# Performance work log

Hardware: AMD Instinct MI355X
Metric: run time of the kernel (lower is better)

Reference implementation:

```python
import jax, jax.numpy as jnp
import numpy as np

N_NODES = 100_000
N_EDGES = 1_250_000
IN_CH = 64
HID = 64
OUT_CH = 10
K = 5
NUM_GRAPHS = 64


def setup_inputs() -> dict:
    key = jax.random.key(0)
    ks = jax.random.split(key, 8)
    x = jax.random.normal(ks[0], (N_NODES, IN_CH), dtype=jnp.float32)
    edge_index = jax.random.randint(ks[1], (2, N_EDGES), 0, N_NODES)
    batch = jnp.sort(jax.random.randint(ks[2], (N_NODES,), 0, NUM_GRAPHS))
    s_in = float(1.0 / np.sqrt(IN_CH))
    s_h = float(1.0 / np.sqrt(HID))
    W1 = jax.random.uniform(ks[3], (K, IN_CH, HID), minval=-s_in, maxval=s_in, dtype=jnp.float32)
    b1 = jnp.zeros((HID,), jnp.float32)
    W2 = jax.random.uniform(ks[4], (K, HID, HID), minval=-s_h, maxval=s_h, dtype=jnp.float32)
    b2 = jnp.zeros((HID,), jnp.float32)
    Wfc = jax.random.uniform(ks[5], (HID, OUT_CH), minval=-s_h, maxval=s_h, dtype=jnp.float32)
    bfc = jnp.zeros((OUT_CH,), jnp.float32)
    return dict(x=x, edge_index=edge_index, batch=batch,
                W1=W1, b1=b1, W2=W2, b2=b2, Wfc=Wfc, bfc=bfc)


def _cheb_conv(x, src, dst, W, b):
    """PyG ChebConv with normalization='rw', lambda_max=2.
    L_rw = I - D^{-1} A ; scaled L_hat = 2*L/lambda_max - I = -D^{-1}A
    (self-loop weights cancel to 0), so each hop is a weighted scatter-add."""
    n = x.shape[0]
    deg = jax.ops.segment_sum(jnp.ones((src.shape[0],), x.dtype), src, num_segments=n)
    inv_deg = jnp.where(deg > 0, 1.0 / deg, 0.0)
    ew = -inv_deg[src]  # per-edge weight of L_hat

    def prop(t):  # (L_hat t)[i] = sum_{j->i} ew * t[j]
        return jax.ops.segment_sum(ew[:, None] * t[src], dst, num_segments=n)

    Tx0 = x
    out = Tx0 @ W[0]
    Tx1 = prop(Tx0)
    out = out + Tx1 @ W[1]
    for k in range(2, W.shape[0]):
        Tx2 = 2.0 * prop(Tx1) - Tx0
        out = out + Tx2 @ W[k]
        Tx0, Tx1 = Tx1, Tx2
    return out + b


def reference(x, edge_index, batch, W1, b1, W2, b2, Wfc, bfc):
    src, dst = edge_index[0], edge_index[1]
    h = jax.nn.selu(_cheb_conv(x, src, dst, W1, b1))
    # AlphaDropout is identity at inference
    h = jax.nn.selu(_cheb_conv(h, src, dst, W2, b2))
    g = jax.ops.segment_sum(h, batch, num_segments=NUM_GRAPHS)  # global_add_pool
    return g @ Wfc + bfc
```

## Files before the change

kernel.cpp:

```cpp
#include <hip/hip_runtime.h>
#include <cstdint>

#define CH 64
#define NBLK 256
#define NBMAX 1024
#define SRCMASK 0x1FFFFu

typedef __attribute__((ext_vector_type(8))) short bf16x8;
typedef __attribute__((ext_vector_type(8))) unsigned short u16x8;
typedef __attribute__((ext_vector_type(4))) float f32x4;
typedef unsigned int uint32;
typedef unsigned char uchar;

__device__ __forceinline__ unsigned short f2bf(float x) {
  unsigned u = __float_as_uint(x);
  u += 0x7FFF + ((u >> 16) & 1);
  return (unsigned short)(u >> 16);
}
__device__ __forceinline__ float bflo(uint32 u) { return __uint_as_float(u << 16); }
__device__ __forceinline__ float bfhi(uint32 u) { return __uint_as_float(u & 0xFFFF0000u); }
__device__ __forceinline__ uint32 bfpack(float lo, float hi) {
  return ((uint32)f2bf(hi) << 16) | (uint32)f2bf(lo);
}

__global__ __launch_bounds__(256) void k_b1(const int* __restrict__ src, const int* __restrict__ dst,
                                            int* __restrict__ cntD, int* __restrict__ cntS, int E, int NB) {
  __shared__ int hD[NBMAX], hS[NBMAX];
  int t = threadIdx.x, b = blockIdx.x;
  for (int i = t; i < NBMAX; i += 256) { hD[i] = 0; hS[i] = 0; }
  __syncthreads();
  int chunk = (E + NBLK - 1) / NBLK;
  int e0 = b * chunk, e1 = min(E, e0 + chunk);
  for (int e = e0 + t; e < e1; e += 256) {
    atomicAdd(&hD[dst[e] >> 7], 1);
    atomicAdd(&hS[src[e] >> 7], 1);
  }
  __syncthreads();
  for (int i = t; i < NB; i += 256) {
    cntD[i * NBLK + b] = hD[i];
    cntS[i * NBLK + b] = hS[i];
  }
}

__global__ __launch_bounds__(256) void k_scan_local(const int* __restrict__ in, int* __restrict__ out,
                                                    int* __restrict__ bsum, int total) {
  __shared__ int s[256];
  int t = threadIdx.x;
  int base = blockIdx.x * 1024 + t * 4;
  int v0 = (base + 0 < total) ? in[base + 0] : 0;
  int v1 = (base + 1 < total) ? in[base + 1] : 0;
  int v2 = (base + 2 < total) ? in[base + 2] : 0;
  int v3 = (base + 3 < total) ? in[base + 3] : 0;
  int sum = v0 + v1 + v2 + v3;
  s[t] = sum;
  __syncthreads();
  for (int off = 1; off < 256; off <<= 1) {
    int x = (t >= off) ? s[t - off] : 0;
    __syncthreads();
    s[t] += x;
    __syncthreads();
  }
  int excl = s[t] - sum;
  if (base + 0 < total) out[base + 0] = excl;  excl += v0;
  if (base + 1 < total) out[base + 1] = excl;  excl += v1;
  if (base + 2 < total) out[base + 2] = excl;  excl += v2;
  if (base + 3 < total) out[base + 3] = excl;
  if (t == 255) bsum[blockIdx.x] = s[255];
}

__global__ __launch_bounds__(256) void k_scan_bsums(int* bsum, int nb) {
  __shared__ int s[256];
  int t = threadIdx.x;
  int v = (t < nb) ? bsum[t] : 0;
  s[t] = v;
  __syncthreads();
  for (int off = 1; off < 256; off <<= 1) {
    int x = (t >= off) ? s[t - off] : 0;
    __syncthreads();
    s[t] += x;
    __syncthreads();
  }
  if (t < nb) bsum[t] = s[t] - v;
}

__global__ __launch_bounds__(256) void k_scan_add(int* __restrict__ arr, const int* __restrict__ bsum, int total) {
  int i = blockIdx.x * 256 + threadIdx.x;
  if (i < total) arr[i] += bsum[i >> 10];
}

__global__ __launch_bounds__(256) void k_b2(const int* __restrict__ src, const int* __restrict__ dst,
                                            const int* __restrict__ cbaseD, const int* __restrict__ cbaseS,
                                            uint32* __restrict__ etmp, uchar* __restrict__ svals, int E, int NB) {
  __shared__ int curD[NBMAX], curS[NBMAX];
  int t = threadIdx.x, b = blockIdx.x;
  for (int i = t; i < NB; i += 256) {
    curD[i] = cbaseD[i * NBLK + b];
    curS[i] = cbaseS[i * NBLK + b];
  }
  __syncthreads();
  int chunk = (E + NBLK - 1) / NBLK;
  int e0 = b * chunk, e1 = min(E, e0 + chunk);
  for (int e = e0 + t; e < e1; e += 256) {
    int s = src[e], d = dst[e];
    int pd = atomicAdd(&curD[d >> 7], 1);
    etmp[pd] = ((uint32)(d & 127) << 17) | (uint32)s;
    int ps = atomicAdd(&curS[s >> 7], 1);
    svals[ps] = (uchar)(s & 127);
  }
}

__global__ __launch_bounds__(256) void k_b3_deg(const uchar* __restrict__ svals, const int* __restrict__ cbaseS,
                                                float* __restrict__ neg_inv, int n, int E, int NB) {
  __shared__ int h[128];
  int t = threadIdx.x, k = blockIdx.x;
  if (t < 128) h[t] = 0;
  __syncthreads();
  int lo = cbaseS[k * NBLK];
  int hi = (k + 1 < NB) ? cbaseS[(k + 1) * NBLK] : E;
  for (int e = lo + t; e < hi; e += 256) atomicAdd(&h[svals[e]], 1);
  __syncthreads();
  if (t < 128) {
    int node = k * 128 + t;
    if (node < n) {
      int c = h[t];
      neg_inv[node] = c > 0 ? (-1.0f / (float)c) : 0.0f;
    }
  }
}

__global__ __launch_bounds__(256) void k_b3_dst(const uint32* __restrict__ etmp, const int* __restrict__ cbaseD,
                                                const float* __restrict__ neg_inv, int2* __restrict__ erec,
                                                int* __restrict__ row_ptr, int n, int E, int NB) {
  __shared__ int h[128], sc[128], cur[128];
  int t = threadIdx.x, k = blockIdx.x;
  if (t < 128) h[t] = 0;
  __syncthreads();
  int lo = cbaseD[k * NBLK];
  int hi = (k + 1 < NB) ? cbaseD[(k + 1) * NBLK] : E;
  for (int e = lo + t; e < hi; e += 256) atomicAdd(&h[(etmp[e] >> 17) & 127], 1);
  __syncthreads();
  if (t < 128) sc[t] = h[t];
  __syncthreads();
  for (int off = 1; off < 128; off <<= 1) {
    int x = (t < 128 && t >= off) ? sc[t - off] : 0;
    __syncthreads();
    if (t < 128) sc[t] += x;
    __syncthreads();
  }
  if (t < 128) {
    int excl = sc[t] - h[t];
    cur[t] = excl;
    int node = k * 128 + t;
    if (node < n) row_ptr[node] = lo + excl;
  }
  if (k == NB - 1 && t == 0) row_ptr[n] = E;
  __syncthreads();
  for (int e = lo + t; e < hi; e += 256) {
    uint32 r = etmp[e];
    int s = (int)(r & SRCMASK);
    int pos = atomicAdd(&cur[(r >> 17) & 127], 1);
    erec[lo + pos] = make_int2(s, __float_as_int(neg_inv[s]));
  }
}

__global__ __launch_bounds__(256) void k_cast(const float* __restrict__ x, unsigned short* __restrict__ xb,
                                              int total8) {
  int i = blockIdx.x * 256 + threadIdx.x;
  if (i < total8) {
    const float4* p = (const float4*)(x + (size_t)i * 8);
    float4 v0 = p[0], v1 = p[1];
    u16x8 w;
    w[0] = f2bf(v0.x); w[1] = f2bf(v0.y); w[2] = f2bf(v0.z); w[3] = f2bf(v0.w);
    w[4] = f2bf(v1.x); w[5] = f2bf(v1.y); w[6] = f2bf(v1.z); w[7] = f2bf(v1.w);
    *(u16x8*)(xb + (size_t)i * 8) = w;
  }
}

__global__ __launch_bounds__(256) void k_prop(const int* __restrict__ row_ptr, const int2* __restrict__ erec,
                                              const uint32* __restrict__ t_in,
                                              const uint32* __restrict__ t_sub,
                                              uint32* __restrict__ t_out, int n, int mode) {
  int tid = threadIdx.x;
  int lane = tid & 63;
  int cp = lane & 31;
  int h = lane >> 5;
  int node = blockIdx.x * 8 + ((tid >> 6) << 1) + h;
  bool active = node < n;
  int beg = active ? row_ptr[node] : 0;
  int end = active ? row_ptr[node + 1] : 0;
  float a0 = 0.f, a1 = 0.f, b0 = 0.f, b1 = 0.f, c0 = 0.f, c1 = 0.f, d0 = 0.f, d1 = 0.f;
  float e0a = 0.f, e1a = 0.f, f0 = 0.f, f1 = 0.f, g0 = 0.f, g1 = 0.f, h0 = 0.f, h1 = 0.f;
  int e = beg;
  for (; e + 8 <= end; e += 8) {
    int2 q0 = erec[e + 0]; int2 q1 = erec[e + 1]; int2 q2 = erec[e + 2]; int2 q3 = erec[e + 3];
    int2 q4 = erec[e + 4]; int2 q5 = erec[e + 5]; int2 q6 = erec[e + 6]; int2 q7 = erec[e + 7];
    uint32 u0 = t_in[q0.x * 32 + cp];
    uint32 u1 = t_in[q1.x * 32 + cp];
    uint32 u2 = t_in[q2.x * 32 + cp];
    uint32 u3 = t_in[q3.x * 32 + cp];
    uint32 u4 = t_in[q4.x * 32 + cp];
    uint32 u5 = t_in[q5.x * 32 + cp];
    uint32 u6 = t_in[q6.x * 32 + cp];
    uint32 u7 = t_in[q7.x * 32 + cp];
    float w0 = __int_as_float(q0.y), w1 = __int_as_float(q1.y);
    float w2 = __int_as_float(q2.y), w3 = __int_as_float(q3.y);
    float w4 = __int_as_float(q4.y), w5 = __int_as_float(q5.y);
    float w6 = __int_as_float(q6.y), w7 = __int_as_float(q7.y);
    a0 = fmaf(w0, bflo(u0), a0);   a1 = fmaf(w0, bfhi(u0), a1);
    b0 = fmaf(w1, bflo(u1), b0);   b1 = fmaf(w1, bfhi(u1), b1);
    c0 = fmaf(w2, bflo(u2), c0);   c1 = fmaf(w2, bfhi(u2), c1);
    d0 = fmaf(w3, bflo(u3), d0);   d1 = fmaf(w3, bfhi(u3), d1);
    e0a = fmaf(w4, bflo(u4), e0a); e1a = fmaf(w4, bfhi(u4), e1a);
    f0 = fmaf(w5, bflo(u5), f0);   f1 = fmaf(w5, bfhi(u5), f1);
    g0 = fmaf(w6, bflo(u6), g0);   g1 = fmaf(w6, bfhi(u6), g1);
    h0 = fmaf(w7, bflo(u7), h0);   h1 = fmaf(w7, bfhi(u7), h1);
  }
  if (e + 4 <= end) {
    int2 q0 = erec[e + 0]; int2 q1 = erec[e + 1]; int2 q2 = erec[e + 2]; int2 q3 = erec[e + 3];
    uint32 u0 = t_in[q0.x * 32 + cp];
    uint32 u1 = t_in[q1.x * 32 + cp];
    uint32 u2 = t_in[q2.x * 32 + cp];
    uint32 u3 = t_in[q3.x * 32 + cp];
    float w0 = __int_as_float(q0.y), w1 = __int_as_float(q1.y);
    float w2 = __int_as_float(q2.y), w3 = __int_as_float(q3.y);
    a0 = fmaf(w0, bflo(u0), a0);   a1 = fmaf(w0, bfhi(u0), a1);
    b0 = fmaf(w1, bflo(u1), b0);   b1 = fmaf(w1, bfhi(u1), b1);
    c0 = fmaf(w2, bflo(u2), c0);   c1 = fmaf(w2, bfhi(u2), c1);
    d0 = fmaf(w3, bflo(u3), d0);   d1 = fmaf(w3, bfhi(u3), d1);
    e += 4;
  }
  if (e + 2 <= end) {
    int2 q0 = erec[e + 0]; int2 q1 = erec[e + 1];
    uint32 u0 = t_in[q0.x * 32 + cp];
    uint32 u1 = t_in[q1.x * 32 + cp];
    float w0 = __int_as_float(q0.y), w1 = __int_as_float(q1.y);
    a0 = fmaf(w0, bflo(u0), a0);   a1 = fmaf(w0, bfhi(u0), a1);
    b0 = fmaf(w1, bflo(u1), b0);   b1 = fmaf(w1, bfhi(u1), b1);
    e += 2;
  }
  if (e < end) {
    int2 q = erec[e];
    uint32 u = t_in[q.x * 32 + cp];
    float w = __int_as_float(q.y);
    a0 = fmaf(w, bflo(u), a0);
    a1 = fmaf(w, bfhi(u), a1);
  }
  float s0 = ((a0 + b0) + (c0 + d0)) + ((e0a + f0) + (g0 + h0));
  float s1 = ((a1 + b1) + (c1 + d1)) + ((e1a + f1) + (g1 + h1));
  if (active) {
    if (mode == 2) {
      uint32 u = t_sub[(size_t)node * 32 + cp];
      s0 = 2.0f * s0 - bflo(u);
      s1 = 2.0f * s1 - bfhi(u);
    }
    t_out[(size_t)node * 32 + cp] = bfpack(s0, s1);
  }
}

__global__ __launch_bounds__(256) void k_prepW(const float* __restrict__ W, unsigned short* __restrict__ Wt) {
  int o = blockIdx.x * 256 + threadIdx.x;
  if (o < 64 * 320) {
    int j = o / 320, k = o - j * 320;
    Wt[o] = f2bf(W[k * 64 + j]);
  }
}

__device__ __forceinline__ float selu(float v) {
  const float sc = 1.0507009873554805f, al = 1.6732632423543773f;
  return (v > 0.f) ? (sc * v) : (sc * al * (expf(v) - 1.f));
}

__global__ __launch_bounds__(256) void k_gemm5(
    const unsigned short* __restrict__ M0, const unsigned short* __restrict__ M1,
    const unsigned short* __restrict__ M2, const unsigned short* __restrict__ M3,
    const unsigned short* __restrict__ M4,
    const unsigned short* __restrict__ Wt, const float* __restrict__ bias,
    unsigned short* __restrict__ outp, int n) {
  __shared__ unsigned short lds[32 * 320];
  const int t = threadIdx.x;
  const int lane = t & 63, wave = t >> 6;
  const int node0 = blockIdx.x * 32;
  const unsigned short* mats[5] = {M0, M1, M2, M3, M4};
#pragma unroll
  for (int m = 0; m < 5; ++m) {
    int row = t >> 3;
    int cc = t & 7;
    int ca = m * 8 + cc;
    u16x8 w = {};
    if (node0 + row < n)
      w = *(const u16x8*)(mats[m] + (size_t)(node0 + row) * CH + cc * 8);
    *(u16x8*)(&lds[row * 320 + ((ca ^ (row & 7)) << 3)]) = w;
  }
  __syncthreads();
  const int g = lane >> 4, r16 = lane & 15;
  const int rowA0 = r16, rowA1 = r16 + 16;
  const int colB = wave * 16 + r16;
  f32x4 acc0 = {}, acc1 = {};
#pragma unroll 2
  for (int kk = 0; kk < 10; ++kk) {
    int ca = kk * 4 + g;
    bf16x8 a0 = *(const bf16x8*)(&lds[rowA0 * 320 + ((ca ^ (rowA0 & 7)) << 3)]);
    bf16x8 a1 = *(const bf16x8*)(&lds[rowA1 * 320 + ((ca ^ (rowA1 & 7)) << 3)]);
    bf16x8 b = *(const bf16x8*)(Wt + colB * 320 + kk * 32 + g * 8);
    acc0 = __builtin_amdgcn_mfma_f32_16x16x32_bf16(a0, b, acc0, 0, 0, 0);
    acc1 = __builtin_amdgcn_mfma_f32_16x16x32_bf16(a1, b, acc1, 0, 0, 0);
  }
  const f32x4 accs[2] = {acc0, acc1};
  int col = wave * 16 + r16;
  float bv = bias[col];
#pragma unroll
  for (int i = 0; i < 2; ++i) {
#pragma unroll
    for (int rr = 0; rr < 4; ++rr) {
      int row = node0 + i * 16 + g * 4 + rr;
      if (row < n)
        outp[(size_t)row * CH + col] = f2bf(selu(accs[i][rr] + bv));
    }
  }
}

__global__ __launch_bounds__(256) void k_gemm5_pool(
    const unsigned short* __restrict__ M0, const unsigned short* __restrict__ M1,
    const unsigned short* __restrict__ M2, const unsigned short* __restrict__ M3,
    const unsigned short* __restrict__ M4,
    const unsigned short* __restrict__ Wt, const float* __restrict__ bias,
    const int* __restrict__ batch, float* __restrict__ gout, int n) {
  __shared__ unsigned short lds[32 * 320];
  const int t = threadIdx.x;
  const int lane = t & 63, wave = t >> 6;
  const int node0 = blockIdx.x * 32;
  const unsigned short* mats[5] = {M0, M1, M2, M3, M4};
#pragma unroll
  for (int m = 0; m < 5; ++m) {
    int row = t >> 3;
    int cc = t & 7;
    int ca = m * 8 + cc;
    u16x8 w = {};
    if (node0 + row < n)
      w = *(const u16x8*)(mats[m] + (size_t)(node0 + row) * CH + cc * 8);
    *(u16x8*)(&lds[row * 320 + ((ca ^ (row & 7)) << 3)]) = w;
  }
  __syncthreads();
  const int g = lane >> 4, r16 = lane & 15;
  const int rowA0 = r16, rowA1 = r16 + 16;
  const int colB = wave * 16 + r16;
  f32x4 acc0 = {}, acc1 = {};
#pragma unroll 2
  for (int kk = 0; kk < 10; ++kk) {
    int ca = kk * 4 + g;
    bf16x8 a0 = *(const bf16x8*)(&lds[rowA0 * 320 + ((ca ^ (rowA0 & 7)) << 3)]);
    bf16x8 a1 = *(const bf16x8*)(&lds[rowA1 * 320 + ((ca ^ (rowA1 & 7)) << 3)]);
    bf16x8 b = *(const bf16x8*)(Wt + colB * 320 + kk * 32 + g * 8);
    acc0 = __builtin_amdgcn_mfma_f32_16x16x32_bf16(a0, b, acc0, 0, 0, 0);
    acc1 = __builtin_amdgcn_mfma_f32_16x16x32_bf16(a1, b, acc1, 0, 0, 0);
  }
  __syncthreads();
  float* S = (float*)lds;
  const f32x4 accs[2] = {acc0, acc1};
  {
    int col = wave * 16 + r16;
    float bv = bias[col];
#pragma unroll
    for (int i = 0; i < 2; ++i)
#pragma unroll
      for (int rr = 0; rr < 4; ++rr) {
        int row = i * 16 + g * 4 + rr;
        S[row * 65 + col] = selu(accs[i][rr] + bv);
      }
  }
  __syncthreads();
  int c = t & 63, w = t >> 6;
  float cur = 0.f;
  int curg = -1;
  for (int r = 0; r < 8; ++r) {
    int row = w * 8 + r;
    int gn = node0 + row;
    if (gn >= n) break;
    int b = batch[gn];
    if (b != curg) {
      if (curg >= 0) atomicAdd(&gout[curg * CH + c], cur);
      curg = b;
      cur = 0.f;
    }
    cur += S[row * 65 + c];
  }
  if (curg >= 0) atomicAdd(&gout[curg * CH + c], cur);
}

__global__ __launch_bounds__(256) void k_fc(const float* __restrict__ g, const float* __restrict__ Wfc,
                                            const float* __restrict__ bfc, float* __restrict__ outp,
                                            int ng, int oc) {
  int i = blockIdx.x * 256 + threadIdx.x;
  if (i < ng * oc) {
    int gi = i / oc, o = i - gi * oc;
    float s = bfc[o];
    for (int ci = 0; ci < CH; ++ci) s += g[gi * CH + ci] * Wfc[ci * oc + o];
    outp[i] = s;
  }
}

extern "C" void kernel_launch(void* const* d_in, const int* in_sizes, int n_in,
                              void* d_out, int out_size, void* d_ws, size_t ws_size,
                              hipStream_t stream) {
  const float* x   = (const float*)d_in[0];
  const int* eidx  = (const int*)d_in[1];
  const int* batch = (const int*)d_in[2];
  const float* W1  = (const float*)d_in[3];
  const float* b1  = (const float*)d_in[4];
  const float* W2  = (const float*)d_in[5];
  const float* b2  = (const float*)d_in[6];
  const float* Wfc = (const float*)d_in[7];
  const float* bfc = (const float*)d_in[8];
  float* out = (float*)d_out;

  const int n  = in_sizes[0] / CH;
  const int E  = in_sizes[1] / 2;
  const int OC = in_sizes[8];
  const int NG = out_size / OC;
  const int NB = (n + 127) >> 7;

  const int* src = eidx;
  const int* dst = eidx + E;

  size_t off = 0;
  char* base = (char*)d_ws;
  auto alloc = [&](size_t bytes) -> void* {
    size_t cur = (off + 255) & ~(size_t)255;
    off = cur + bytes;
    return (void*)(base + cur);
  };
  const int scan_total = NB * NBLK;
  const int scan_nb    = (scan_total + 1023) / 1024;
  int*   cntD   = (int*)alloc((size_t)scan_total * 4);
  int*   cntS   = (int*)alloc((size_t)scan_total * 4);
  int*   bsumD  = (int*)alloc((size_t)scan_nb * 4);
  int*   bsumS  = (int*)alloc((size_t)scan_nb * 4);
  float* neg_inv = (float*)alloc((size_t)n * 4);
  int*   row_ptr = (int*)alloc((size_t)(n + 1) * 4);
  int2*  erec    = (int2*)alloc((size_t)E * 8);
  const size_t tb16 = (size_t)n * CH * 2;
  unsigned short* Xb = (unsigned short*)alloc(tb16);
  unsigned short* T1 = (unsigned short*)alloc(tb16);
  unsigned short* T2 = (unsigned short*)alloc(tb16);
  unsigned short* T3 = (unsigned short*)alloc(tb16);
  unsigned short* T4 = (unsigned short*)alloc(tb16);
  unsigned short* H  = (unsigned short*)alloc(tb16);
  uint32* etmp  = (uint32*)alloc((size_t)E * 4);
  uchar*  svals = (uchar*)alloc((size_t)E);
  float* g  = (float*)alloc((size_t)NG * CH * 4);
  unsigned short* Wt1 = (unsigned short*)alloc(64 * 320 * 2);
  unsigned short* Wt2 = (unsigned short*)alloc(64 * 320 * 2);
  if (off > ws_size) return;

  hipMemsetAsync(g, 0, (size_t)NG * CH * 4, stream);

  k_b1<<<NBLK, 256, 0, stream>>>(src, dst, cntD, cntS, E, NB);
  k_scan_local<<<scan_nb, 256, 0, stream>>>(cntD, cntD, bsumD, scan_total);
  k_scan_bsums<<<1, 256, 0, stream>>>(bsumD, scan_nb);
  k_scan_add<<<(scan_total + 255) / 256, 256, 0, stream>>>(cntD, bsumD, scan_total);
  k_scan_local<<<scan_nb, 256, 0, stream>>>(cntS, cntS, bsumS, scan_total);
  k_scan_bsums<<<1, 256, 0, stream>>>(bsumS, scan_nb);
  k_scan_add<<<(scan_total + 255) / 256, 256, 0, stream>>>(cntS, bsumS, scan_total);
  k_b2<<<NBLK, 256, 0, stream>>>(src, dst, cntD, cntS, etmp, svals, E, NB);
  k_b3_deg<<<NB, 256, 0, stream>>>(svals, cntS, neg_inv, n, E, NB);
  k_b3_dst<<<NB, 256, 0, stream>>>(etmp, cntD, neg_inv, erec, row_ptr, n, E, NB);

  k_prepW<<<80, 256, 0, stream>>>(W1, Wt1);
  k_prepW<<<80, 256, 0, stream>>>(W2, Wt2);
  k_cast<<<(n * CH / 8 + 255) / 256, 256, 0, stream>>>(x, Xb, n * CH / 8);

  const int pb = (n + 7) / 8;
  const int gb = (n + 31) / 32;
  k_prop<<<pb, 256, 0, stream>>>(row_ptr, erec, (const uint32*)Xb, nullptr, (uint32*)T1, n, 1);
  k_prop<<<pb, 256, 0, stream>>>(row_ptr, erec, (const uint32*)T1, (const uint32*)Xb, (uint32*)T2, n, 2);
  k_prop<<<pb, 256, 0, stream>>>(row_ptr, erec, (const uint32*)T2, (const uint32*)T1, (uint32*)T3, n, 2);
  k_prop<<<pb, 256, 0, stream>>>(row_ptr, erec, (const uint32*)T3, (const uint32*)T2, (uint32*)T4, n, 2);
  k_gemm5<<<gb, 256, 0, stream>>>(Xb, T1, T2, T3, T4, Wt1, b1, H, n);
  k_prop<<<pb, 256, 0, stream>>>(row_ptr, erec, (const uint32*)H,  nullptr, (uint32*)T1, n, 1);
  k_prop<<<pb, 256, 0, stream>>>(row_ptr, erec, (const uint32*)T1, (const uint32*)H,  (uint32*)T2, n, 2);
  k_prop<<<pb, 256, 0, stream>>>(row_ptr, erec, (const uint32*)T2, (const uint32*)T1, (uint32*)T3, n, 2);
  k_prop<<<pb, 256, 0, stream>>>(row_ptr, erec, (const uint32*)T3, (const uint32*)T2, (uint32*)T4, n, 2);
  k_gemm5_pool<<<gb, 256, 0, stream>>>(H, T1, T2, T3, T4, Wt2, b2, batch, g, n);
  k_fc<<<(NG * OC + 255) / 256, 256, 0, stream>>>(g, Wfc, bfc, out, NG, OC);
}
```

Measured before the change: 417.9 us.

## Process propagation nodes in degree-sorted order for wavefront load balance

Adds a counting sort of nodes by in-degree (histogram, scan, scatter) and has the propagation kernel look up its node through this permutation, so the two nodes sharing a wavefront and the nodes sharing a block have similar edge counts. The aim is to cut divergence and tail imbalance in the eight propagation passes. The cost is three extra small kernels plus a memset, an indirection load per node, and loss of locality in the output writes and row_ptr reads. Within a degree bucket, the atomic scatter leaves node order nondeterministic.

```diff
diff --git a/kernel.cpp b/kernel.cpp
--- a/kernel.cpp
+++ b/kernel.cpp
@@ -163,6 +163,43 @@
   }
 }
 
+__global__ __launch_bounds__(256) void k_deg_hist(const int* __restrict__ row_ptr, int* __restrict__ hist, int n) {
+  __shared__ int h[256];
+  int t = threadIdx.x;
+  h[t] = 0;
+  __syncthreads();
+  for (int i = blockIdx.x * 256 + t; i < n; i += gridDim.x * 256) {
+    int d = min(row_ptr[i + 1] - row_ptr[i], 255);
+    atomicAdd(&h[255 - d], 1);
+  }
+  __syncthreads();
+  if (h[t]) atomicAdd(&hist[t], h[t]);
+}
+
+__global__ __launch_bounds__(256) void k_deg_scan(int* hist) {
+  __shared__ int s[256];
+  int t = threadIdx.x;
+  int v = hist[t];
+  s[t] = v;
+  __syncthreads();
+  for (int off = 1; off < 256; off <<= 1) {
+    int x = (t >= off) ? s[t - off] : 0;
+    __syncthreads();
+    s[t] += x;
+    __syncthreads();
+  }
+  hist[t] = s[t] - v;
+}
+
+__global__ __launch_bounds__(256) void k_deg_scatter(const int* __restrict__ row_ptr, int* __restrict__ hist,
+                                                     int* __restrict__ perm, int n) {
+  for (int i = blockIdx.x * 256 + threadIdx.x; i < n; i += gridDim.x * 256) {
+    int d = min(row_ptr[i + 1] - row_ptr[i], 255);
+    int pos = atomicAdd(&hist[255 - d], 1);
+    perm[pos] = i;
+  }
+}
+
 __global__ __launch_bounds__(256) void k_cast(const float* __restrict__ x, unsigned short* __restrict__ xb,
                                               int total8) {
   int i = blockIdx.x * 256 + threadIdx.x;
@@ -177,6 +214,7 @@
 }
 
 __global__ __launch_bounds__(256) void k_prop(const int* __restrict__ row_ptr, const int2* __restrict__ erec,
+                                              const int* __restrict__ perm,
                                               const uint32* __restrict__ t_in,
                                               const uint32* __restrict__ t_sub,
                                               uint32* __restrict__ t_out, int n, int mode) {
@@ -184,8 +222,9 @@
   int lane = tid & 63;
   int cp = lane & 31;
   int h = lane >> 5;
-  int node = blockIdx.x * 8 + ((tid >> 6) << 1) + h;
-  bool active = node < n;
+  int slot = blockIdx.x * 8 + ((tid >> 6) << 1) + h;
+  bool active = slot < n;
+  int node = active ? perm[slot] : 0;
   int beg = active ? row_ptr[node] : 0;
   int end = active ? row_ptr[node + 1] : 0;
   float a0 = 0.f, a1 = 0.f, b0 = 0.f, b1 = 0.f, c0 = 0.f, c1 = 0.f, d0 = 0.f, d1 = 0.f;
@@ -438,6 +477,8 @@
   float* neg_inv = (float*)alloc((size_t)n * 4);
   int*   row_ptr = (int*)alloc((size_t)(n + 1) * 4);
   int2*  erec    = (int2*)alloc((size_t)E * 8);
+  int*   perm    = (int*)alloc((size_t)n * 4);
+  int*   dhist   = (int*)alloc(256 * 4);
   const size_t tb16 = (size_t)n * CH * 2;
   unsigned short* Xb = (unsigned short*)alloc(tb16);
   unsigned short* T1 = (unsigned short*)alloc(tb16);
@@ -453,6 +494,7 @@
   if (off > ws_size) return;
 
   hipMemsetAsync(g, 0, (size_t)NG * CH * 4, stream);
+  hipMemsetAsync(dhist, 0, 256 * 4, stream);
 
   k_b1<<<NBLK, 256, 0, stream>>>(src, dst, cntD, cntS, E, NB);
   k_scan_local<<<scan_nb, 256, 0, stream>>>(cntD, cntD, bsumD, scan_total);
@@ -464,6 +506,9 @@
   k_b2<<<NBLK, 256, 0, stream>>>(src, dst, cntD, cntS, etmp, svals, E, NB);
   k_b3_deg<<<NB, 256, 0, stream>>>(svals, cntS, neg_inv, n, E, NB);
   k_b3_dst<<<NB, 256, 0, stream>>>(etmp, cntD, neg_inv, erec, row_ptr, n, E, NB);
+  k_deg_hist<<<256, 256, 0, stream>>>(row_ptr, dhist, n);
+  k_deg_scan<<<1, 256, 0, stream>>>(dhist);
+  k_deg_scatter<<<256, 256, 0, stream>>>(row_ptr, dhist, perm, n);
 
   k_prepW<<<80, 256, 0, stream>>>(W1, Wt1);
   k_prepW<<<80, 256, 0, stream>>>(W2, Wt2);
@@ -471,15 +516,15 @@
 
   const int pb = (n + 7) / 8;
   const int gb = (n + 31) / 32;
-  k_prop<<<pb, 256, 0, stream>>>(row_ptr, erec, (const uint32*)Xb, nullptr, (uint32*)T1, n, 1);
-  k_prop<<<pb, 256, 0, stream>>>(row_ptr, erec, (const uint32*)T1, (const uint32*)Xb, (uint32*)T2, n, 2);
-  k_prop<<<pb, 256, 0, stream>>>(row_ptr, erec, (const uint32*)T2, (const uint32*)T1, (uint32*)T3, n, 2);
-  k_prop<<<pb, 256, 0, stream>>>(row_ptr, erec, (const uint32*)T3, (const uint32*)T2, (uint32*)T4, n, 2);
+  k_prop<<<pb, 256, 0, stream>>>(row_ptr, erec, perm, (const uint32*)Xb, nullptr, (uint32*)T1, n, 1);
+  k_prop<<<pb, 256, 0, stream>>>(row_ptr, erec, perm, (const uint32*)T1, (const uint32*)Xb, (uint32*)T2, n, 2);
+  k_prop<<<pb, 256, 0, stream>>>(row_ptr, erec, perm, (const uint32*)T2, (const uint32*)T1, (uint32*)T3, n, 2);
+  k_prop<<<pb, 256, 0, stream>>>(row_ptr, erec, perm, (const uint32*)T3, (const uint32*)T2, (uint32*)T4, n, 2);
   k_gemm5<<<gb, 256, 0, stream>>>(Xb, T1, T2, T3, T4, Wt1, b1, H, n);
-  k_prop<<<pb, 256, 0, stream>>>(row_ptr, erec, (const uint32*)H,  nullptr, (uint32*)T1, n, 1);
-  k_prop<<<pb, 256, 0, stream>>>(row_ptr, erec, (const uint32*)T1, (const uint32*)H,  (uint32*)T2, n, 2);
-  k_prop<<<pb, 256, 0, stream>>>(row_ptr, erec, (const uint32*)T2, (const uint32*)T1, (uint32*)T3, n, 2);
-  k_prop<<<pb, 256, 0, stream>>>(row_ptr, erec, (const uint32*)T3, (const uint32*)T2, (uint32*)T4, n, 2);
+  k_prop<<<pb, 256, 0, stream>>>(row_ptr, erec, perm, (const uint32*)H,  nullptr, (uint32*)T1, n, 1);
+  k_prop<<<pb, 256, 0, stream>>>(row_ptr, erec, perm, (const uint32*)T1, (const uint32*)H,  (uint32*)T2, n, 2);
+  k_prop<<<pb, 256, 0, stream>>>(row_ptr, erec, perm, (const uint32*)T2, (const uint32*)T1, (uint32*)T3, n, 2);
+  k_prop<<<pb, 256, 0, stream>>>(row_ptr, erec, perm, (const uint32*)T3, (const uint32*)T2, (uint32*)T4, n, 2);
   k_gemm5_pool<<<gb, 256, 0, stream>>>(H, T1, T2, T3, T4, Wt2, b2, batch, g, n);
   k_fc<<<(NG * OC + 255) / 256, 256, 0, stream>>>(g, Wfc, bfc, out, NG, OC);
 }
```

Measured after the change: 725.0 us. 1.73x slower.

## Make GEMM kernels persistent with double-buffered LDS and register-resident weights

Applied to the files above, without the earlier changes.

Both Chebyshev GEMM kernels become persistent grid-stride loops over 32-node strips, with at most 1024 blocks. Each wave loads its weight fragments into registers once, and the next strip's five input matrices are loaded into a second LDS buffer while the current strip's MFMAs run. This aims to cut per-block setup cost, avoid re-reading weights every strip, and overlap global loads with compute. In exchange it uses more registers and twice the LDS, which can lower occupancy, and the GEMMs are a small share of total time next to the eight propagation passes.

```diff
diff --git a/kernel.cpp b/kernel.cpp
--- a/kernel.cpp
+++ b/kernel.cpp
@@ -275,47 +275,72 @@
     const unsigned short* __restrict__ M2, const unsigned short* __restrict__ M3,
     const unsigned short* __restrict__ M4,
     const unsigned short* __restrict__ Wt, const float* __restrict__ bias,
-    unsigned short* __restrict__ outp, int n) {
-  __shared__ unsigned short lds[32 * 320];
+    unsigned short* __restrict__ outp, int n, int nstrips) {
+  __shared__ unsigned short lds[2][32 * 320];
   const int t = threadIdx.x;
   const int lane = t & 63, wave = t >> 6;
-  const int node0 = blockIdx.x * 32;
+  const int g = lane >> 4, r16 = lane & 15;
   const unsigned short* mats[5] = {M0, M1, M2, M3, M4};
-#pragma unroll
-  for (int m = 0; m < 5; ++m) {
-    int row = t >> 3;
-    int cc = t & 7;
-    int ca = m * 8 + cc;
-    u16x8 w = {};
-    if (node0 + row < n)
-      w = *(const u16x8*)(mats[m] + (size_t)(node0 + row) * CH + cc * 8);
-    *(u16x8*)(&lds[row * 320 + ((ca ^ (row & 7)) << 3)]) = w;
-  }
-  __syncthreads();
-  const int g = lane >> 4, r16 = lane & 15;
-  const int rowA0 = r16, rowA1 = r16 + 16;
   const int colB = wave * 16 + r16;
-  f32x4 acc0 = {}, acc1 = {};
-#pragma unroll 2
-  for (int kk = 0; kk < 10; ++kk) {
-    int ca = kk * 4 + g;
-    bf16x8 a0 = *(const bf16x8*)(&lds[rowA0 * 320 + ((ca ^ (rowA0 & 7)) << 3)]);
-    bf16x8 a1 = *(const bf16x8*)(&lds[rowA1 * 320 + ((ca ^ (rowA1 & 7)) << 3)]);
-    bf16x8 b = *(const bf16x8*)(Wt + colB * 320 + kk * 32 + g * 8);
-    acc0 = __builtin_amdgcn_mfma_f32_16x16x32_bf16(a0, b, acc0, 0, 0, 0);
-    acc1 = __builtin_amdgcn_mfma_f32_16x16x32_bf16(a1, b, acc1, 0, 0, 0);
-  }
-  const f32x4 accs[2] = {acc0, acc1};
-  int col = wave * 16 + r16;
-  float bv = bias[col];
-#pragma unroll
-  for (int i = 0; i < 2; ++i) {
-#pragma unroll
-    for (int rr = 0; rr < 4; ++rr) {
-      int row = node0 + i * 16 + g * 4 + rr;
-      if (row < n)
-        outp[(size_t)row * CH + col] = f2bf(selu(accs[i][rr] + bv));
-    }
+  bf16x8 Bf[10];
+#pragma unroll
+  for (int kk = 0; kk < 10; ++kk)
+    Bf[kk] = *(const bf16x8*)(Wt + colB * 320 + kk * 32 + g * 8);
+  const float bv = bias[colB];
+  const int srow = t >> 3, scc = t & 7;
+
+  int strip = blockIdx.x;
+  if (strip >= nstrips) return;
+  int cur = 0;
+  {
+    int node0 = strip * 32;
+#pragma unroll
+    for (int m = 0; m < 5; ++m) {
+      int ca = m * 8 + scc;
+      u16x8 w = {};
+      if (node0 + srow < n)
+        w = *(const u16x8*)(mats[m] + (size_t)(node0 + srow) * CH + scc * 8);
+      *(u16x8*)(&lds[0][srow * 320 + ((ca ^ (srow & 7)) << 3)]) = w;
+    }
+  }
+  __syncthreads();
+  for (; strip < nstrips; strip += gridDim.x) {
+    int nxt = strip + gridDim.x;
+    if (nxt < nstrips) {
+      int node0 = nxt * 32;
+#pragma unroll
+      for (int m = 0; m < 5; ++m) {
+        int ca = m * 8 + scc;
+        u16x8 w = {};
+        if (node0 + srow < n)
+          w = *(const u16x8*)(mats[m] + (size_t)(node0 + srow) * CH + scc * 8);
+        *(u16x8*)(&lds[cur ^ 1][srow * 320 + ((ca ^ (srow & 7)) << 3)]) = w;
+      }
+    }
+    const unsigned short* L = lds[cur];
+    const int rowA0 = r16, rowA1 = r16 + 16;
+    f32x4 acc0 = {}, acc1 = {};
+#pragma unroll
+    for (int kk = 0; kk < 10; ++kk) {
+      int ca = kk * 4 + g;
+      bf16x8 a0 = *(const bf16x8*)(&L[rowA0 * 320 + ((ca ^ (rowA0 & 7)) << 3)]);
+      bf16x8 a1 = *(const bf16x8*)(&L[rowA1 * 320 + ((ca ^ (rowA1 & 7)) << 3)]);
+      acc0 = __builtin_amdgcn_mfma_f32_16x16x32_bf16(a0, Bf[kk], acc0, 0, 0, 0);
+      acc1 = __builtin_amdgcn_mfma_f32_16x16x32_bf16(a1, Bf[kk], acc1, 0, 0, 0);
+    }
+    int node0 = strip * 32;
+    const f32x4 accs[2] = {acc0, acc1};
+#pragma unroll
+    for (int i = 0; i < 2; ++i) {
+#pragma unroll
+      for (int rr = 0; rr < 4; ++rr) {
+        int row = node0 + i * 16 + g * 4 + rr;
+        if (row < n)
+          outp[(size_t)row * CH + colB] = f2bf(selu(accs[i][rr] + bv));
+      }
+    }
+    __syncthreads();
+    cur ^= 1;
   }
 }
 
@@ -324,67 +349,90 @@
     const unsigned short* __restrict__ M2, const unsigned short* __restrict__ M3,
     const unsigned short* __restrict__ M4,
     const unsigned short* __restrict__ Wt, const float* __restrict__ bias,
-    const int* __restrict__ batch, float* __restrict__ gout, int n) {
-  __shared__ unsigned short lds[32 * 320];
+    const int* __restrict__ batch, float* __restrict__ gout, int n, int nstrips) {
+  __shared__ unsigned short lds[2][32 * 320];
   const int t = threadIdx.x;
   const int lane = t & 63, wave = t >> 6;
-  const int node0 = blockIdx.x * 32;
+  const int g = lane >> 4, r16 = lane & 15;
   const unsigned short* mats[5] = {M0, M1, M2, M3, M4};
-#pragma unroll
-  for (int m = 0; m < 5; ++m) {
-    int row = t >> 3;
-    int cc = t & 7;
-    int ca = m * 8 + cc;
-    u16x8 w = {};
-    if (node0 + row < n)
-      w = *(const u16x8*)(mats[m] + (size_t)(node0 + row) * CH + cc * 8);
-    *(u16x8*)(&lds[row * 320 + ((ca ^ (row & 7)) << 3)]) = w;
-  }
-  __syncthreads();
-  const int g = lane >> 4, r16 = lane & 15;
-  const int rowA0 = r16, rowA1 = r16 + 16;
   const int colB = wave * 16 + r16;
-  f32x4 acc0 = {}, acc1 = {};
-#pragma unroll 2
-  for (int kk = 0; kk < 10; ++kk) {
-    int ca = kk * 4 + g;
-    bf16x8 a0 = *(const bf16x8*)(&lds[rowA0 * 320 + ((ca ^ (rowA0 & 7)) << 3)]);
-    bf16x8 a1 = *(const bf16x8*)(&lds[rowA1 * 320 + ((ca ^ (rowA1 & 7)) << 3)]);
-    bf16x8 b = *(const bf16x8*)(Wt + colB * 320 + kk * 32 + g * 8);
-    acc0 = __builtin_amdgcn_mfma_f32_16x16x32_bf16(a0, b, acc0, 0, 0, 0);
-    acc1 = __builtin_amdgcn_mfma_f32_16x16x32_bf16(a1, b, acc1, 0, 0, 0);
-  }
-  __syncthreads();
-  float* S = (float*)lds;
-  const f32x4 accs[2] = {acc0, acc1};
+  bf16x8 Bf[10];
+#pragma unroll
+  for (int kk = 0; kk < 10; ++kk)
+    Bf[kk] = *(const bf16x8*)(Wt + colB * 320 + kk * 32 + g * 8);
+  const float bv = bias[colB];
+  const int srow = t >> 3, scc = t & 7;
+
+  int strip = blockIdx.x;
+  if (strip >= nstrips) return;
+  int cur = 0;
   {
-    int col = wave * 16 + r16;
-    float bv = bias[col];
+    int node0 = strip * 32;
+#pragma unroll
+    for (int m = 0; m < 5; ++m) {
+      int ca = m * 8 + scc;
+      u16x8 w = {};
+      if (node0 + srow < n)
+        w = *(const u16x8*)(mats[m] + (size_t)(node0 + srow) * CH + scc * 8);
+      *(u16x8*)(&lds[0][srow * 320 + ((ca ^ (srow & 7)) << 3)]) = w;
+    }
+  }
+  __syncthreads();
+  for (; strip < nstrips; strip += gridDim.x) {
+    int nxt = strip + gridDim.x;
+    if (nxt < nstrips) {
+      int node0 = nxt * 32;
+#pragma unroll
+      for (int m = 0; m < 5; ++m) {
+        int ca = m * 8 + scc;
+        u16x8 w = {};
+        if (node0 + srow < n)
+          w = *(const u16x8*)(mats[m] + (size_t)(node0 + srow) * CH + scc * 8);
+        *(u16x8*)(&lds[cur ^ 1][srow * 320 + ((ca ^ (srow & 7)) << 3)]) = w;
+      }
+    }
+    const unsigned short* L = lds[cur];
+    const int rowA0 = r16, rowA1 = r16 + 16;
+    f32x4 acc0 = {}, acc1 = {};
+#pragma unroll
+    for (int kk = 0; kk < 10; ++kk) {
+      int ca = kk * 4 + g;
+      bf16x8 a0 = *(const bf16x8*)(&L[rowA0 * 320 + ((ca ^ (rowA0 & 7)) << 3)]);
+      bf16x8 a1 = *(const bf16x8*)(&L[rowA1 * 320 + ((ca ^ (rowA1 & 7)) << 3)]);
+      acc0 = __builtin_amdgcn_mfma_f32_16x16x32_bf16(a0, Bf[kk], acc0, 0, 0, 0);
+      acc1 = __builtin_amdgcn_mfma_f32_16x16x32_bf16(a1, Bf[kk], acc1, 0, 0, 0);
+    }
+    __syncthreads();
+    float* S = (float*)lds[cur];
+    const f32x4 accs[2] = {acc0, acc1};
 #pragma unroll
     for (int i = 0; i < 2; ++i)
 #pragma unroll
       for (int rr = 0; rr < 4; ++rr) {
         int row = i * 16 + g * 4 + rr;
-        S[row * 65 + col] = selu(accs[i][rr] + bv);
+        S[row * 65 + colB] = selu(accs[i][rr] + bv);
       }
-  }
-  __syncthreads();
-  int c = t & 63, w = t >> 6;
-  float cur = 0.f;
-  int curg = -1;
-  for (int r = 0; r < 8; ++r) {
-    int row = w * 8 + r;
-    int gn = node0 + row;
-    if (gn >= n) break;
-    int b = batch[gn];
-    if (b != curg) {
-      if (curg >= 0) atomicAdd(&gout[curg * CH + c], cur);
-      curg = b;
-      cur = 0.f;
-    }
-    cur += S[row * 65 + c];
-  }
-  if (curg >= 0) atomicAdd(&gout[curg * CH + c], cur);
+    __syncthreads();
+    int node0 = strip * 32;
+    int c = t & 63, w = t >> 6;
+    float curv = 0.f;
+    int curg = -1;
+    for (int r = 0; r < 8; ++r) {
+      int row = w * 8 + r;
+      int gn = node0 + row;
+      if (gn >= n) break;
+      int b = batch[gn];
+      if (b != curg) {
+        if (curg >= 0) atomicAdd(&gout[curg * CH + c], curv);
+        curg = b;
+        curv = 0.f;
+      }
+      curv += S[row * 65 + c];
+    }
+    if (curg >= 0) atomicAdd(&gout[curg * CH + c], curv);
+    __syncthreads();
+    cur ^= 1;
+  }
 }
 
 __global__ __launch_bounds__(256) void k_fc(const float* __restrict__ g, const float* __restrict__ Wfc,
@@ -470,16 +518,17 @@
   k_cast<<<(n * CH / 8 + 255) / 256, 256, 0, stream>>>(x, Xb, n * CH / 8);
 
   const int pb = (n + 7) / 8;
-  const int gb = (n + 31) / 32;
+  const int nstrips = (n + 31) / 32;
+  const int gb = nstrips < 1024 ? nstrips : 1024;
   k_prop<<<pb, 256, 0, stream>>>(row_ptr, erec, (const uint32*)Xb, nullptr, (uint32*)T1, n, 1);
   k_prop<<<pb, 256, 0, stream>>>(row_ptr, erec, (const uint32*)T1, (const uint32*)Xb, (uint32*)T2, n, 2);
   k_prop<<<pb, 256, 0, stream>>>(row_ptr, erec, (const uint32*)T2, (const uint32*)T1, (uint32*)T3, n, 2);
   k_prop<<<pb, 256, 0, stream>>>(row_ptr, erec, (const uint32*)T3, (const uint32*)T2, (uint32*)T4, n, 2);
-  k_gemm5<<<gb, 256, 0, stream>>>(Xb, T1, T2, T3, T4, Wt1, b1, H, n);
+  k_gemm5<<<gb, 256, 0, stream>>>(Xb, T1, T2, T3, T4, Wt1, b1, H, n, nstrips);
   k_prop<<<pb, 256, 0, stream>>>(row_ptr, erec, (const uint32*)H,  nullptr, (uint32*)T1, n, 1);
   k_prop<<<pb, 256, 0, stream>>>(row_ptr, erec, (const uint32*)T1, (const uint32*)H,  (uint32*)T2, n, 2);
   k_prop<<<pb, 256, 0, stream>>>(row_ptr, erec, (const uint32*)T2, (const uint32*)T1, (uint32*)T3, n, 2);
   k_prop<<<pb, 256, 0, stream>>>(row_ptr, erec, (const uint32*)T3, (const uint32*)T2, (uint32*)T4, n, 2);
-  k_gemm5_pool<<<gb, 256, 0, stream>>>(H, T1, T2, T3, T4, Wt2, b2, batch, g, n);
+  k_gemm5_pool<<<gb, 256, 0, stream>>>(H, T1, T2, T3, T4, Wt2, b2, batch, g, n, nstrips);
   k_fc<<<(NG * OC + 255) / 256, 256, 0, stream>>>(g, Wfc, bfc, out, NG, OC);
 }
```

New measurement: 398.7 us. -4.6%, faster.
